# Optimization experiments

Measured on AMD Instinct MI355X. Metric: run time of the kernel, lower is better.

Reference implementation:

```python
import jax, jax.numpy as jnp
import numpy as np

B, R, N, D_IN, D_OUT = 8, 8, 1024, 256, 256


def setup_inputs() -> dict:
    key = jax.random.key(0)
    k1, k2, k3, k4 = jax.random.split(key, 4)
    x = jax.random.normal(k1, (B, N, D_IN), dtype=jnp.float32)
    adj_stack = jax.random.uniform(k2, (B, R, N, N), dtype=jnp.float32)
    # per-relation Linear params, stacked: W[r] maps D_IN -> D_OUT
    bound = 1.0 / np.sqrt(D_IN)
    W = jax.random.uniform(k3, (R, D_IN, D_OUT), minval=-bound, maxval=bound, dtype=jnp.float32)
    b = jax.random.uniform(k4, (R, D_OUT), minval=-bound, maxval=bound, dtype=jnp.float32)
    return {"x": x, "adj_stack": adj_stack, "W": W, "b": b}


def reference(x, adj_stack, W, b):
    # support[b,r,n,e] = x[b,n,:] @ W[r] + b[r]
    support = jnp.einsum('bnd,rde->brne', x, W) + b[None, :, None, :]
    # out[b,m,e] = sum_r adj[b,r,m,:] @ support[b,r,:,e]
    out = jnp.einsum('brmn,brne->bme', adj_stack, support)
    return jax.nn.relu(out)
```

## Files before the change

### kernel.cpp

```cpp
#include <hip/hip_runtime.h>
#include <hip/hip_bf16.h>


#define Bb 8
#define Rr 8
#define Nn 1024
#define Dd 256

typedef __attribute__((ext_vector_type(8))) short short8;
typedef __attribute__((ext_vector_type(4))) short short4v;
typedef __attribute__((ext_vector_type(4))) float f32x4;

__device__ __forceinline__ short f2bf(float f) {
    unsigned u = __builtin_bit_cast(unsigned, f);
    u += 0x7fffu + ((u >> 16) & 1u);
    return (short)(u >> 16);
}

__global__ __launch_bounds__(256, 2) void support_kernel(
        const float* __restrict__ x, const float* __restrict__ W,
        const float* __restrict__ bias, short* __restrict__ sup) {
    __shared__ short As[128][40];
    __shared__ short Bs[128][40];

    const int tid = threadIdx.x;
    const int e_t = blockIdx.x;
    const int n_t = blockIdx.y;
    const int br  = blockIdx.z;
    const int b   = br >> 3, r = br & 7;

    const int wave = tid >> 6, lane = tid & 63;
    const int quad = lane >> 4, l16 = lane & 15;
    const int we = wave & 1, wn = wave >> 1;

    f32x4 acc[4][4] = {};

    const float* Wr = W + r * Dd * Dd;
    const float* xb = x + ((size_t)b * Nn + n_t * 128) * Dd;

    for (int d0 = 0; d0 < Dd; d0 += 32) {
        #pragma unroll
        for (int i = 0; i < 4; ++i) {
            int idx = tid + i * 256;
            int d_l = idx >> 5;
            int e_l = (idx & 31) * 4;
            f32x4 v = *(const f32x4*)(Wr + (d0 + d_l) * Dd + e_t * 128 + e_l);
            As[e_l + 0][d_l] = f2bf(v[0]);
            As[e_l + 1][d_l] = f2bf(v[1]);
            As[e_l + 2][d_l] = f2bf(v[2]);
            As[e_l + 3][d_l] = f2bf(v[3]);
        }
        #pragma unroll
        for (int i = 0; i < 4; ++i) {
            int idx = tid + i * 256;
            int n_l = idx >> 3;
            int d4  = (idx & 7) * 4;
            f32x4 v = *(const f32x4*)(xb + n_l * Dd + d0 + d4);
            short4v s;
            s[0] = f2bf(v[0]); s[1] = f2bf(v[1]); s[2] = f2bf(v[2]); s[3] = f2bf(v[3]);
            *(short4v*)&Bs[n_l][d4] = s;
        }
        __syncthreads();
        short8 a[4], bf[4];
        #pragma unroll
        for (int i = 0; i < 4; ++i)
            a[i] = *(const short8*)&As[we * 64 + i * 16 + l16][quad * 8];
        #pragma unroll
        for (int j = 0; j < 4; ++j)
            bf[j] = *(const short8*)&Bs[wn * 64 + j * 16 + l16][quad * 8];
        #pragma unroll
        for (int i = 0; i < 4; ++i)
            #pragma unroll
            for (int j = 0; j < 4; ++j)
                acc[i][j] = __builtin_amdgcn_mfma_f32_16x16x32_bf16(a[i], bf[j], acc[i][j], 0, 0, 0);
        __syncthreads();
    }

    #pragma unroll
    for (int i = 0; i < 4; ++i) {
        #pragma unroll
        for (int reg = 0; reg < 4; ++reg) {
            int e = e_t * 128 + we * 64 + i * 16 + quad * 4 + reg;
            float bv = bias[r * Dd + e];
            #pragma unroll
            for (int j = 0; j < 4; ++j) {
                int n = n_t * 128 + wn * 64 + j * 16 + l16;
                sup[(((b * Rr + r) * Dd + e) << 10) + n] = f2bf(acc[i][j][reg] + bv);
            }
        }
    }
}

__global__ __launch_bounds__(256, 2) void gcn_gemm_kernel(
        const float* __restrict__ adj, const short* __restrict__ sup,
        float* __restrict__ out) {
    __shared__ short Aa[128][40];
    __shared__ short Bs[128][40];

    const int tid = threadIdx.x;
    const int e2  = blockIdx.x & 1;
    const int ks  = blockIdx.x >> 1;
    const int m_t = blockIdx.y;
    const int b   = blockIdx.z;

    const int wave = tid >> 6, lane = tid & 63;
    const int quad = lane >> 4, l16 = lane & 15;
    const int wm = wave >> 1, we = wave & 1;

    f32x4 acc[4][4] = {};

    for (int it = 0; it < 64; ++it) {
        const int kk = ks * 2048 + it * 32;
        const int r  = kk >> 10;
        const int n0 = kk & 1023;

        const float* ap = adj + ((size_t)((b * Rr + r) * Nn + m_t * 128)) * Nn + n0;
        #pragma unroll
        for (int i = 0; i < 4; ++i) {
            int idx = tid + i * 256;
            int m_l = idx >> 3;
            int k4  = (idx & 7) * 4;
            f32x4 v = *(const f32x4*)(ap + (size_t)m_l * Nn + k4);
            short4v s;
            s[0] = f2bf(v[0]); s[1] = f2bf(v[1]); s[2] = f2bf(v[2]); s[3] = f2bf(v[3]);
            *(short4v*)&Aa[m_l][k4] = s;
        }
        const short* bp = sup + (((size_t)((b * Rr + r) * Dd + e2 * 128)) << 10) + n0;
        #pragma unroll
        for (int i = 0; i < 2; ++i) {
            int idx = tid + i * 256;
            int e_l = idx >> 2;
            int k8  = (idx & 3) * 8;
            short8 v = *(const short8*)(bp + ((size_t)e_l << 10) + k8);
            *(short8*)&Bs[e_l][k8] = v;
        }
        __syncthreads();
        short8 a[4], bf[4];
        #pragma unroll
        for (int i = 0; i < 4; ++i)
            a[i] = *(const short8*)&Aa[wm * 64 + i * 16 + l16][quad * 8];
        #pragma unroll
        for (int j = 0; j < 4; ++j)
            bf[j] = *(const short8*)&Bs[we * 64 + j * 16 + l16][quad * 8];
        #pragma unroll
        for (int i = 0; i < 4; ++i)
            #pragma unroll
            for (int j = 0; j < 4; ++j)
                acc[i][j] = __builtin_amdgcn_mfma_f32_16x16x32_bf16(a[i], bf[j], acc[i][j], 0, 0, 0);
        __syncthreads();
    }

    float* ob = out + ((size_t)b * Nn + m_t * 128) * Dd + e2 * 128;
    #pragma unroll
    for (int i = 0; i < 4; ++i)
        #pragma unroll
        for (int reg = 0; reg < 4; ++reg) {
            int m_l = wm * 64 + i * 16 + quad * 4 + reg;
            #pragma unroll
            for (int j = 0; j < 4; ++j) {
                int e_l = we * 64 + j * 16 + l16;
                atomicAdd(ob + (size_t)m_l * Dd + e_l, acc[i][j][reg]);
            }
        }
}

__global__ void relu_kernel(float* __restrict__ out, int n4) {
    int i = blockIdx.x * blockDim.x + threadIdx.x;
    if (i < n4) {
        f32x4* p = (f32x4*)out;
        f32x4 v = p[i];
        v[0] = fmaxf(v[0], 0.f); v[1] = fmaxf(v[1], 0.f);
        v[2] = fmaxf(v[2], 0.f); v[3] = fmaxf(v[3], 0.f);
        p[i] = v;
    }
}

extern "C" void kernel_launch(void* const* d_in, const int* in_sizes, int n_in,
                              void* d_out, int out_size, void* d_ws, size_t ws_size,
                              hipStream_t stream) {
    const float* x    = (const float*)d_in[0];
    const float* adj  = (const float*)d_in[1];
    const float* W    = (const float*)d_in[2];
    const float* bias = (const float*)d_in[3];
    float* out = (float*)d_out;
    short* sup = (short*)d_ws;

    hipMemsetAsync(d_out, 0, (size_t)out_size * sizeof(float), stream);
    support_kernel<<<dim3(2, 8, 64), 256, 0, stream>>>(x, W, bias, sup);
    gcn_gemm_kernel<<<dim3(8, 8, 8), 256, 0, stream>>>(adj, sup, out);
    relu_kernel<<<(out_size / 4 + 255) / 256, 256, 0, stream>>>(out, out_size / 4);
}
```

Baseline: 537.9 us.

## Prefetch tiles into registers, pre-transpose W to bf16, split K per relation

Adds a prep kernel that converts W to bf16 and transposes it once into the output buffer, used as scratch before the memset. Both GEMM kernels now prefetch the next K-tile into registers while the current tile is staged in shared memory and multiplied. The adjacency GEMM grid doubles so each block handles one relation's K range, which raises parallelism but doubles the atomic adds into the output. Launch-bounds occupancy hints are dropped, which may raise register use.

Result: faster. 464.7 us (-13.6%).

```diff
diff --git a/kernel.cpp b/kernel.cpp
--- a/kernel.cpp
+++ b/kernel.cpp
@@ -17,67 +17,99 @@
     return (short)(u >> 16);
 }
 
-__global__ __launch_bounds__(256, 2) void support_kernel(
-        const float* __restrict__ x, const float* __restrict__ W,
+__global__ void prep_w_kernel(const float* __restrict__ W, short* __restrict__ Wt) {
+    __shared__ short T[64][72];
+    const int tid = threadIdx.x;
+    const int et = blockIdx.x, dt = blockIdx.y, r = blockIdx.z;
+    const float* Wr = W + ((size_t)r * Dd + dt * 64) * Dd + et * 64;
+    #pragma unroll
+    for (int i = 0; i < 4; ++i) {
+        int idx = tid + i * 256;
+        int d_l = idx >> 4;
+        int e4  = (idx & 15) * 4;
+        f32x4 v = *(const f32x4*)(Wr + d_l * Dd + e4);
+        T[e4 + 0][d_l] = f2bf(v[0]);
+        T[e4 + 1][d_l] = f2bf(v[1]);
+        T[e4 + 2][d_l] = f2bf(v[2]);
+        T[e4 + 3][d_l] = f2bf(v[3]);
+    }
+    __syncthreads();
+    short* o = Wt + ((size_t)r * Dd + et * 64) * Dd + dt * 64;
+    #pragma unroll
+    for (int i = 0; i < 2; ++i) {
+        int idx = tid + i * 256;
+        int e_l = idx >> 3;
+        int d8  = (idx & 7) * 8;
+        *(short8*)(o + e_l * Dd + d8) = *(const short8*)&T[e_l][d8];
+    }
+}
+
+__global__ __launch_bounds__(256) void support_kernel(
+        const float* __restrict__ x, const short* __restrict__ Wt,
         const float* __restrict__ bias, short* __restrict__ sup) {
     __shared__ short As[128][40];
     __shared__ short Bs[128][40];
 
     const int tid = threadIdx.x;
-    const int e_t = blockIdx.x;
-    const int n_t = blockIdx.y;
-    const int br  = blockIdx.z;
-    const int b   = br >> 3, r = br & 7;
-
+    const int e_t = blockIdx.x, n_t = blockIdx.y, br = blockIdx.z;
+    const int b = br >> 3, r = br & 7;
     const int wave = tid >> 6, lane = tid & 63;
     const int quad = lane >> 4, l16 = lane & 15;
     const int we = wave & 1, wn = wave >> 1;
 
+    const short* wp = Wt + ((size_t)r * Dd + e_t * 128) * Dd;
+    const float* xb = x + ((size_t)b * Nn + n_t * 128) * Dd;
+
+    short8 aw[2];
+    f32x4 xv[4];
+    auto load = [&](int d0) {
+        #pragma unroll
+        for (int i = 0; i < 2; ++i) {
+            int idx = tid + i * 256;
+            aw[i] = *(const short8*)(wp + (idx >> 2) * Dd + d0 + (idx & 3) * 8);
+        }
+        #pragma unroll
+        for (int i = 0; i < 4; ++i) {
+            int idx = tid + i * 256;
+            xv[i] = *(const f32x4*)(xb + (idx >> 3) * Dd + d0 + (idx & 7) * 4);
+        }
+    };
+
     f32x4 acc[4][4] = {};
-
-    const float* Wr = W + r * Dd * Dd;
-    const float* xb = x + ((size_t)b * Nn + n_t * 128) * Dd;
-
-    for (int d0 = 0; d0 < Dd; d0 += 32) {
-        #pragma unroll
-        for (int i = 0; i < 4; ++i) {
-            int idx = tid + i * 256;
-            int d_l = idx >> 5;
-            int e_l = (idx & 31) * 4;
-            f32x4 v = *(const f32x4*)(Wr + (d0 + d_l) * Dd + e_t * 128 + e_l);
-            As[e_l + 0][d_l] = f2bf(v[0]);
-            As[e_l + 1][d_l] = f2bf(v[1]);
-            As[e_l + 2][d_l] = f2bf(v[2]);
-            As[e_l + 3][d_l] = f2bf(v[3]);
-        }
-        #pragma unroll
-        for (int i = 0; i < 4; ++i) {
-            int idx = tid + i * 256;
-            int n_l = idx >> 3;
-            int d4  = (idx & 7) * 4;
-            f32x4 v = *(const f32x4*)(xb + n_l * Dd + d0 + d4);
+    load(0);
+    for (int it = 0; it < 8; ++it) {
+        #pragma unroll
+        for (int i = 0; i < 2; ++i) {
+            int idx = tid + i * 256;
+            *(short8*)&As[idx >> 2][(idx & 3) * 8] = aw[i];
+        }
+        #pragma unroll
+        for (int i = 0; i < 4; ++i) {
+            int idx = tid + i * 256;
             short4v s;
-            s[0] = f2bf(v[0]); s[1] = f2bf(v[1]); s[2] = f2bf(v[2]); s[3] = f2bf(v[3]);
-            *(short4v*)&Bs[n_l][d4] = s;
-        }
-        __syncthreads();
-        short8 a[4], bf[4];
+            s[0] = f2bf(xv[i][0]); s[1] = f2bf(xv[i][1]);
+            s[2] = f2bf(xv[i][2]); s[3] = f2bf(xv[i][3]);
+            *(short4v*)&Bs[idx >> 3][(idx & 7) * 4] = s;
+        }
+        if (it < 7) load((it + 1) * 32);
+        __syncthreads();
+        short8 a[4], bfr[4];
         #pragma unroll
         for (int i = 0; i < 4; ++i)
             a[i] = *(const short8*)&As[we * 64 + i * 16 + l16][quad * 8];
         #pragma unroll
         for (int j = 0; j < 4; ++j)
-            bf[j] = *(const short8*)&Bs[wn * 64 + j * 16 + l16][quad * 8];
+            bfr[j] = *(const short8*)&Bs[wn * 64 + j * 16 + l16][quad * 8];
         #pragma unroll
         for (int i = 0; i < 4; ++i)
             #pragma unroll
             for (int j = 0; j < 4; ++j)
-                acc[i][j] = __builtin_amdgcn_mfma_f32_16x16x32_bf16(a[i], bf[j], acc[i][j], 0, 0, 0);
-        __syncthreads();
-    }
-
-    #pragma unroll
-    for (int i = 0; i < 4; ++i) {
+                acc[i][j] = __builtin_amdgcn_mfma_f32_16x16x32_bf16(a[i], bfr[j], acc[i][j], 0, 0, 0);
+        __syncthreads();
+    }
+
+    #pragma unroll
+    for (int i = 0; i < 4; ++i)
         #pragma unroll
         for (int reg = 0; reg < 4; ++reg) {
             int e = e_t * 128 + we * 64 + i * 16 + quad * 4 + reg;
@@ -88,10 +120,9 @@
                 sup[(((b * Rr + r) * Dd + e) << 10) + n] = f2bf(acc[i][j][reg] + bv);
             }
         }
-    }
-}
-
-__global__ __launch_bounds__(256, 2) void gcn_gemm_kernel(
+}
+
+__global__ __launch_bounds__(256) void gcn_gemm_kernel(
         const float* __restrict__ adj, const short* __restrict__ sup,
         float* __restrict__ out) {
     __shared__ short Aa[128][40];
@@ -99,54 +130,60 @@
 
     const int tid = threadIdx.x;
     const int e2  = blockIdx.x & 1;
-    const int ks  = blockIdx.x >> 1;
-    const int m_t = blockIdx.y;
-    const int b   = blockIdx.z;
-
+    const int r   = blockIdx.x >> 1;
+    const int m_t = blockIdx.y, b = blockIdx.z;
     const int wave = tid >> 6, lane = tid & 63;
     const int quad = lane >> 4, l16 = lane & 15;
     const int wm = wave >> 1, we = wave & 1;
 
+    const float* ap = adj + ((size_t)((b * Rr + r) * Nn + m_t * 128)) * Nn;
+    const short* bp = sup + (((size_t)((b * Rr + r) * Dd + e2 * 128)) << 10);
+
+    f32x4 av[4];
+    short8 bv[2];
+    auto load = [&](int n0) {
+        #pragma unroll
+        for (int i = 0; i < 4; ++i) {
+            int idx = tid + i * 256;
+            av[i] = *(const f32x4*)(ap + (size_t)(idx >> 3) * Nn + n0 + (idx & 7) * 4);
+        }
+        #pragma unroll
+        for (int i = 0; i < 2; ++i) {
+            int idx = tid + i * 256;
+            bv[i] = *(const short8*)(bp + ((size_t)(idx >> 2) << 10) + n0 + (idx & 3) * 8);
+        }
+    };
+
     f32x4 acc[4][4] = {};
-
-    for (int it = 0; it < 64; ++it) {
-        const int kk = ks * 2048 + it * 32;
-        const int r  = kk >> 10;
-        const int n0 = kk & 1023;
-
-        const float* ap = adj + ((size_t)((b * Rr + r) * Nn + m_t * 128)) * Nn + n0;
-        #pragma unroll
-        for (int i = 0; i < 4; ++i) {
-            int idx = tid + i * 256;
-            int m_l = idx >> 3;
-            int k4  = (idx & 7) * 4;
-            f32x4 v = *(const f32x4*)(ap + (size_t)m_l * Nn + k4);
+    load(0);
+    for (int it = 0; it < 32; ++it) {
+        #pragma unroll
+        for (int i = 0; i < 4; ++i) {
+            int idx = tid + i * 256;
             short4v s;
-            s[0] = f2bf(v[0]); s[1] = f2bf(v[1]); s[2] = f2bf(v[2]); s[3] = f2bf(v[3]);
-            *(short4v*)&Aa[m_l][k4] = s;
-        }
-        const short* bp = sup + (((size_t)((b * Rr + r) * Dd + e2 * 128)) << 10) + n0;
-        #pragma unroll
-        for (int i = 0; i < 2; ++i) {
-            int idx = tid + i * 256;
-            int e_l = idx >> 2;
-            int k8  = (idx & 3) * 8;
-            short8 v = *(const short8*)(bp + ((size_t)e_l << 10) + k8);
-            *(short8*)&Bs[e_l][k8] = v;
-        }
-        __syncthreads();
-        short8 a[4], bf[4];
+            s[0] = f2bf(av[i][0]); s[1] = f2bf(av[i][1]);
+            s[2] = f2bf(av[i][2]); s[3] = f2bf(av[i][3]);
+            *(short4v*)&Aa[idx >> 3][(idx & 7) * 4] = s;
+        }
+        #pragma unroll
+        for (int i = 0; i < 2; ++i) {
+            int idx = tid + i * 256;
+            *(short8*)&Bs[idx >> 2][(idx & 3) * 8] = bv[i];
+        }
+        if (it < 31) load((it + 1) * 32);
+        __syncthreads();
+        short8 a[4], bfr[4];
         #pragma unroll
         for (int i = 0; i < 4; ++i)
             a[i] = *(const short8*)&Aa[wm * 64 + i * 16 + l16][quad * 8];
         #pragma unroll
         for (int j = 0; j < 4; ++j)
-            bf[j] = *(const short8*)&Bs[we * 64 + j * 16 + l16][quad * 8];
+            bfr[j] = *(const short8*)&Bs[we * 64 + j * 16 + l16][quad * 8];
         #pragma unroll
         for (int i = 0; i < 4; ++i)
             #pragma unroll
             for (int j = 0; j < 4; ++j)
-                acc[i][j] = __builtin_amdgcn_mfma_f32_16x16x32_bf16(a[i], bf[j], acc[i][j], 0, 0, 0);
+                acc[i][j] = __builtin_amdgcn_mfma_f32_16x16x32_bf16(a[i], bfr[j], acc[i][j], 0, 0, 0);
         __syncthreads();
     }
 
@@ -184,9 +221,11 @@
     const float* bias = (const float*)d_in[3];
     float* out = (float*)d_out;
     short* sup = (short*)d_ws;
-
+    short* Wt  = (short*)d_out;
+
+    prep_w_kernel<<<dim3(4, 4, 8), 256, 0, stream>>>(W, Wt);
+    support_kernel<<<dim3(2, 8, 64), 256, 0, stream>>>(x, Wt, bias, sup);
     hipMemsetAsync(d_out, 0, (size_t)out_size * sizeof(float), stream);
-    support_kernel<<<dim3(2, 8, 64), 256, 0, stream>>>(x, W, bias, sup);
-    gcn_gemm_kernel<<<dim3(8, 8, 8), 256, 0, stream>>>(adj, sup, out);
+    gcn_gemm_kernel<<<dim3(16, 8, 8), 256, 0, stream>>>(adj, sup, out);
     relu_kernel<<<(out_size / 4 + 255) / 256, 256, 0, stream>>>(out, out_size / 4);
 }
```
